# Optimization experiments

Hardware: AMD Instinct MI355X
Metric: run time of the kernel (lower is better)

Reference implementation:

```python
import jax, jax.numpy as jnp
import numpy as np

S, B, E, H = 2048, 4, 1024, 16
HD = E // H
EPS = 1e-8


def _bit_linear(x, W, b):
    """BitNetLinear (eval): ternary weight quant + abs-mean activation scaling."""
    w_scale = jnp.maximum(jnp.mean(jnp.abs(W)), EPS)
    wn = W / w_scale
    qw = jnp.sign(wn) * (jnp.abs(wn) > 0.5).astype(x.dtype)  # {-1,0,1}
    a_scale = jnp.maximum(jnp.mean(jnp.abs(x)), EPS)
    out = (x / a_scale) @ (qw * w_scale).T + b
    return out * a_scale


def setup_inputs() -> dict:
    key = jax.random.key(0)
    ks = jax.random.split(key, 9)
    # xavier-uniform-ish init for [E,E] weights
    lim = float(np.sqrt(6.0 / (E + E)))
    def w(k):
        return jax.random.uniform(k, (E, E), jnp.float32, -lim, lim)
    return {
        "query": jax.random.normal(ks[0], (S, B, E), jnp.float32),
        "Wq": w(ks[1]), "bq": jnp.zeros((E,), jnp.float32),
        "Wk": w(ks[2]), "bk": jnp.zeros((E,), jnp.float32),
        "Wv": w(ks[3]), "bv": jnp.zeros((E,), jnp.float32),
        "Wo": w(ks[4]), "bo": jnp.zeros((E,), jnp.float32),
    }


def reference(query, Wq, bq, Wk, bk, Wv, bv, Wo, bo):
    q = _bit_linear(query, Wq, bq)  # [S,B,E]
    k = _bit_linear(query, Wk, bk)
    v = _bit_linear(query, Wv, bv)
    # [S,B,E] -> [B*H, S, HD]
    def split_heads(t):
        return t.reshape(S, B * H, HD).transpose(1, 0, 2)
    q, k, v = split_heads(q), split_heads(k), split_heads(v)
    scaling = HD ** -0.5
    scores = jnp.einsum("nqd,nkd->nqk", q, k) * scaling  # [B*H,S,S]
    probs = jax.nn.softmax(scores, axis=-1)
    attn = jnp.einsum("nqk,nkd->nqd", probs, v)  # [B*H,S,HD]
    attn = attn.transpose(1, 0, 2).reshape(S, B, E)
    out = _bit_linear(attn, Wo, bo)  # [S,B,E]
    # need_weights=True, average_attn_weights=True -> mean over heads
    attn_weights = probs.reshape(B, H, S, S).mean(axis=1)  # [B,S,S]
    return out, attn_weights
```

## Files before the change

### kernel.cpp

```cpp
#include <hip/hip_runtime.h>


typedef __bf16 bf16_t;
typedef __bf16 bf16x8 __attribute__((ext_vector_type(8)));
typedef float  f32x4  __attribute__((ext_vector_type(4)));

#define MFMA16(Af, Bf, Cv) __builtin_amdgcn_mfma_f32_16x16x32_bf16((Af), (Bf), (Cv), 0, 0, 0)
#define EXP2(x) __builtin_amdgcn_exp2f(x)

constexpr float LOG2E   = 1.4426950408889634f;
constexpr float SHIFT2  = 14.426950408889634f;
constexpr float QSCALE  = 0.125f * LOG2E;

__device__ __forceinline__ void gload16(const void* g, void* l) {
  __builtin_amdgcn_global_load_lds(
      (const __attribute__((address_space(1))) void*)g,
      (__attribute__((address_space(3))) void*)l, 16, 0, 0);
}

__device__ __forceinline__ void stage8k(const bf16_t* __restrict__ g0, int gstride,
                                        char* ldsb, int tid, int w) {
  const int rr = tid >> 3;
  const int cs = ((tid & 7) * 8) ^ ((rr & 7) * 8);
  gload16(g0 + (size_t)rr * gstride + cs, ldsb + w * 1024);
  gload16(g0 + (size_t)(rr + 32) * gstride + cs, ldsb + 4096 + w * 1024);
}

__device__ __forceinline__ void stage8k512(const bf16_t* __restrict__ g0, int gstride,
                                           char* ldsb, int tid) {
  const int rr = tid >> 3;
  const int cs = ((tid & 7) * 8) ^ ((rr & 7) * 8);
  gload16(g0 + (size_t)rr * gstride + cs, ldsb + (tid >> 6) * 1024);
}

__device__ __forceinline__ bf16x8 lds_frag(const char* ldsb, int row, int bytecol) {
  return *(const bf16x8*)(ldsb + row * 128 + (bytecol ^ ((row & 7) << 4)));
}

constexpr int S_ = 2048, B_ = 4, E_ = 1024, H_ = 16, HD_ = 64;
constexpr int M_ = S_ * B_;
constexpr int NH_ = B_ * H_;

constexpr size_t OFF_SCALES = 0;
constexpr size_t OFF_PART   = 256;
constexpr size_t OFF_XB     = 8192;
constexpr size_t SZ_X       = (size_t)M_ * E_ * 2;
constexpr size_t OFF_TQKV   = OFF_XB + SZ_X;
constexpr size_t OFF_TO     = OFF_TQKV + (size_t)3072 * 1024 * 2;
constexpr size_t OFF_QH     = OFF_TO + (size_t)1024 * 1024 * 2;
constexpr size_t SZ_HD      = (size_t)NH_ * S_ * HD_ * 2;
constexpr size_t OFF_KH     = OFF_QH + SZ_HD;
constexpr size_t OFF_VT     = OFF_KH + SZ_HD;
constexpr size_t OFF_STL    = OFF_VT + SZ_HD;
constexpr size_t OFF_ATTN   = OFF_STL + (size_t)NH_ * S_ * 4;

__global__ void k_abs_sum_w4(const float4* __restrict__ W0, const float4* __restrict__ W1,
                             const float4* __restrict__ W2, const float4* __restrict__ W3,
                             float* __restrict__ part) {
  const int seg = blockIdx.x >> 8, blk = blockIdx.x & 255;
  const float4* src = (seg == 0) ? W0 : (seg == 1) ? W1 : (seg == 2) ? W2 : W3;
  float s = 0.f;
  for (int i = blk * 256 + threadIdx.x; i < 262144; i += 65536) {
    float4 x = src[i];
    s += fabsf(x.x) + fabsf(x.y) + fabsf(x.z) + fabsf(x.w);
  }
  __shared__ float red[256];
  red[threadIdx.x] = s; __syncthreads();
  for (int st = 128; st > 0; st >>= 1) {
    if (threadIdx.x < st) red[threadIdx.x] += red[threadIdx.x + st];
    __syncthreads();
  }
  if (threadIdx.x == 0) part[seg * 256 + blk] = red[0];
}

__global__ void k_prep_x(const float4* __restrict__ X, ushort4* __restrict__ Xb,
                         float* __restrict__ part) {
  float s = 0.f;
  for (int i = blockIdx.x * 256 + threadIdx.x; i < 2097152; i += 65536) {
    float4 v = X[i];
    s += fabsf(v.x) + fabsf(v.y) + fabsf(v.z) + fabsf(v.w);
    ushort4 h;
    h.x = __builtin_bit_cast(unsigned short, (__bf16)v.x);
    h.y = __builtin_bit_cast(unsigned short, (__bf16)v.y);
    h.z = __builtin_bit_cast(unsigned short, (__bf16)v.z);
    h.w = __builtin_bit_cast(unsigned short, (__bf16)v.w);
    Xb[i] = h;
  }
  __shared__ float red[256];
  red[threadIdx.x] = s; __syncthreads();
  for (int st = 128; st > 0; st >>= 1) {
    if (threadIdx.x < st) red[threadIdx.x] += red[threadIdx.x + st];
    __syncthreads();
  }
  if (threadIdx.x == 0) part[blockIdx.x] = red[0];
}

__global__ void k_abs_sum_bf16(const bf16x8* __restrict__ src, int n8, float* __restrict__ out) {
  float s = 0.f;
  for (int i = blockIdx.x * blockDim.x + threadIdx.x; i < n8; i += gridDim.x * blockDim.x) {
    bf16x8 x = src[i];
    #pragma unroll
    for (int e = 0; e < 8; ++e) s += fabsf((float)x[e]);
  }
  __shared__ float red[256];
  red[threadIdx.x] = s; __syncthreads();
  for (int st = 128; st > 0; st >>= 1) {
    if (threadIdx.x < st) red[threadIdx.x] += red[threadIdx.x + st];
    __syncthreads();
  }
  if (threadIdx.x == 0) out[blockIdx.x] = red[0];
}

__global__ void k_finalize(const float* __restrict__ part, float* __restrict__ scales,
                           int r0, int r1) {
  __shared__ float red[256];
  int t = threadIdx.x;
  for (int r = r0; r < r1; ++r) {
    red[t] = part[r * 256 + t];
    __syncthreads();
    for (int st = 128; st > 0; st >>= 1) {
      if (t < st) red[t] += red[t + st];
      __syncthreads();
    }
    if (t == 0) {
      float cnt = (r < 4) ? 1048576.0f : 8388608.0f;
      scales[r] = fmaxf(red[0] / cnt, 1e-8f);
    }
    __syncthreads();
  }
}

__device__ __forceinline__ unsigned short tern_u(float w, float wsc) {
  float wn = w / wsc;
  if (!(fabsf(wn) > 0.5f)) return 0;
  return (wn > 0.f) ? (unsigned short)0x3F80 : (unsigned short)0xBF80;
}

__global__ void k_quantize4(const float4* __restrict__ W0, const float4* __restrict__ W1,
                            const float4* __restrict__ W2, const float4* __restrict__ W3,
                            const float* __restrict__ scales,
                            ushort4* __restrict__ T0, ushort4* __restrict__ T1,
                            ushort4* __restrict__ T2, ushort4* __restrict__ T3) {
  const int seg = blockIdx.x >> 10;
  const int i = (blockIdx.x & 1023) * 256 + threadIdx.x;
  const float4* W = (seg == 0) ? W0 : (seg == 1) ? W1 : (seg == 2) ? W2 : W3;
  ushort4* T = (seg == 0) ? T0 : (seg == 1) ? T1 : (seg == 2) ? T2 : T3;
  float wsc = scales[seg];
  float4 w = W[i];
  ushort4 o;
  o.x = tern_u(w.x, wsc); o.y = tern_u(w.y, wsc);
  o.z = tern_u(w.z, wsc); o.w = tern_u(w.w, wsc);
  T[i] = o;
}

__global__ __launch_bounds__(256) void k_gemm_qkv(
    const bf16_t* __restrict__ Xb, const bf16_t* __restrict__ T,
    const float* __restrict__ scales,
    const float* __restrict__ bq, const float* __restrict__ bk, const float* __restrict__ bv,
    bf16_t* __restrict__ Qh, bf16_t* __restrict__ Kh, bf16_t* __restrict__ Vt) {
  __shared__ char lds[32768];
  const int tid = threadIdx.x, w = tid >> 6, lane = tid & 63;
  const int g = lane >> 4, cc = lane & 15;
  const int l = blockIdx.x;
  const int xcd = l & 7, r = l >> 3;
  const int nIdx = r % 24, mloc = r / 24;
  const int bm = (xcd * 8 + mloc) * 128, bn = nIdx * 128;
  const int wm = (w >> 1) * 64, wn = (w & 1) * 64;
  const int subA = wm >> 6, subB = wn >> 6;
  f32x4 acc[4][4] = {};
  for (int kt = 0; kt < 16; ++kt) {
    const int k0 = kt * 64;
    const bf16_t* xa = &Xb[(size_t)bm * 1024 + k0];
    const bf16_t* tb = &T[(size_t)bn * 1024 + k0];
    stage8k(xa, 1024, lds, tid, w);
    stage8k(xa + 64 * 1024, 1024, lds + 8192, tid, w);
    stage8k(tb, 1024, lds + 16384, tid, w);
    stage8k(tb + 64 * 1024, 1024, lds + 24576, tid, w);
    __syncthreads();
    const char* As = lds + subA * 8192;
    const char* Bs = lds + 16384 + subB * 8192;
    #pragma unroll
    for (int ks = 0; ks < 2; ++ks) {
      bf16x8 af[4], bfr[4];
      #pragma unroll
      for (int i = 0; i < 4; ++i)
        af[i] = lds_frag(As, (wm & 63) + i * 16 + cc, ks * 64 + g * 16);
      #pragma unroll
      for (int j = 0; j < 4; ++j)
        bfr[j] = lds_frag(Bs, (wn & 63) + j * 16 + cc, ks * 64 + g * 16);
      __builtin_amdgcn_s_setprio(1);
      #pragma unroll
      for (int i = 0; i < 4; ++i)
        #pragma unroll
        for (int j = 0; j < 4; ++j)
          acc[i][j] = MFMA16(af[i], bfr[j], acc[i][j]);
      __builtin_amdgcn_s_setprio(0);
    }
    __syncthreads();
  }
  const int seg = bn >> 10;
  const float wsc = scales[seg];
  const float asx = scales[4];
  const float* bias = (seg == 0) ? bq : (seg == 1) ? bk : bv;
  #pragma unroll
  for (int i = 0; i < 4; ++i)
    #pragma unroll
    for (int j = 0; j < 4; ++j)
      #pragma unroll
      for (int r2 = 0; r2 < 4; ++r2) {
        int m = bm + wm + i * 16 + g * 4 + r2;
        int n = bn + wn + j * 16 + cc;
        int e = n & 1023;
        float v = acc[i][j][r2] * wsc + bias[e] * asx;
        int s = m >> 2, b = m & 3, h = e >> 6, d = e & 63;
        if (seg == 0) {
          Qh[((b * 16 + h) * 2048 + s) * 64 + d] = (bf16_t)(v * QSCALE);
        } else if (seg == 1) {
          Kh[((b * 16 + h) * 2048 + s) * 64 + d] = (bf16_t)v;
        } else {
          Vt[((b * 16 + h) * 64 + d) * 2048 + s] = (bf16_t)v;
        }
      }
}

__global__ __launch_bounds__(512) void k_flash(
    const bf16_t* __restrict__ Qh, const bf16_t* __restrict__ Kh,
    const bf16_t* __restrict__ Vt,
    bf16_t* __restrict__ attnb, float* __restrict__ stl) {
  __shared__ char lds[81920];
  char* Ps = lds + 49152;
  const int tid = threadIdx.x, w = tid >> 6, lane = tid & 63;
  const int g = lane >> 4, cc = lane & 15;
  const int l = blockIdx.x;
  const int head = (l & 7) * 8 + ((l >> 3) & 7);
  const int q0 = (l >> 6) * 256;
  const int qbaseA = (head * 2048 + q0 + w * 32 + cc) * 64 + g * 8;
  const int qbaseB = qbaseA + 16 * 64;
  const bf16x8 qa0 = *(const bf16x8*)&Qh[qbaseA];
  const bf16x8 qa1 = *(const bf16x8*)&Qh[qbaseA + 32];
  const bf16x8 qb0 = *(const bf16x8*)&Qh[qbaseB];
  const bf16x8 qb1 = *(const bf16x8*)&Qh[qbaseB + 32];
  const bf16_t* Kb = Kh + (size_t)head * 2048 * 64;
  const bf16_t* Vb = Vt + (size_t)head * 64 * 2048;
  const bf16_t one_b = (bf16_t)1.0f;
  const bf16x8 ones = {one_b, one_b, one_b, one_b, one_b, one_b, one_b, one_b};
  const f32x4 minit = {-SHIFT2, -SHIFT2, -SHIFT2, -SHIFT2};
  f32x4 accOA[4] = {}, accOB[4] = {};
  f32x4 accLA = {}, accLB = {};
  stage8k512(Kb, 64, lds, tid);
  stage8k512(Vb, 2048, lds + 24576, tid);
  stage8k512(Kb + 64 * 64, 64, lds + 8192, tid);
  stage8k512(Vb + 64, 2048, lds + 24576 + 8192, tid);
  int cur = 0;
  for (int t = 0; t < 32; ++t) {
    if (t < 31) asm volatile("s_waitcnt vmcnt(2)" ::: "memory");
    else        asm volatile("s_waitcnt vmcnt(0)" ::: "memory");
    __builtin_amdgcn_s_barrier();
    if (t + 2 < 32) {
      int nb = cur + 2; if (nb >= 3) nb -= 3;
      stage8k512(Kb + (t + 2) * 64 * 64, 64, lds + nb * 8192, tid);
      stage8k512(Vb + (t + 2) * 64, 2048, lds + 24576 + nb * 8192, tid);
    }
    const char* KhL = lds + cur * 8192;
    const char* VtL = lds + 24576 + cur * 8192;
    f32x4 sA[4], sB[4];
    #pragma unroll
    for (int nf = 0; nf < 4; ++nf) { sA[nf] = minit; sB[nf] = minit; }
    __builtin_amdgcn_s_setprio(1);
    #pragma unroll
    for (int nf = 0; nf < 4; ++nf) {
      const int row = nf * 16 + cc;
      bf16x8 kh0 = lds_frag(KhL, row, g * 16);
      bf16x8 kh1 = lds_frag(KhL, row, 64 + g * 16);
      sA[nf] = MFMA16(qa0, kh0, sA[nf]);
      sA[nf] = MFMA16(qa1, kh1, sA[nf]);
      sB[nf] = MFMA16(qb0, kh0, sB[nf]);
      sB[nf] = MFMA16(qb1, kh1, sB[nf]);
    }
    __builtin_amdgcn_s_setprio(0);
    #pragma unroll
    for (int nf = 0; nf < 4; ++nf)
      #pragma unroll
      for (int r = 0; r < 4; ++r) {
        float pA = EXP2(sA[nf][r]);
        float pB = EXP2(sB[nf][r]);
        int rowA = w * 32 + g * 4 + r;
        int rowB = rowA + 16;
        int colb = (nf * 16 + cc) * 2;
        *(bf16_t*)(Ps + ((rowA * 128 + colb) ^ ((rowA & 7) << 4))) = (bf16_t)pA;
        *(bf16_t*)(Ps + ((rowB * 128 + colb) ^ ((rowB & 7) << 4))) = (bf16_t)pB;
      }
    const int prA = w * 32 + cc, prB = prA + 16;
    const int pbA = (prA * 128 + g * 16) ^ ((prA & 7) << 4);
    const int pbB = (prB * 128 + g * 16) ^ ((prB & 7) << 4);
    const bf16x8 paA0 = *(const bf16x8*)(Ps + pbA);
    const bf16x8 paA1 = *(const bf16x8*)(Ps + (pbA ^ 64));
    const bf16x8 paB0 = *(const bf16x8*)(Ps + pbB);
    const bf16x8 paB1 = *(const bf16x8*)(Ps + (pbB ^ 64));
    __builtin_amdgcn_s_setprio(1);
    accLA = MFMA16(paA0, ones, accLA);
    accLA = MFMA16(paA1, ones, accLA);
    accLB = MFMA16(paB0, ones, accLB);
    accLB = MFMA16(paB1, ones, accLB);
    #pragma unroll
    for (int df = 0; df < 4; ++df) {
      const int row = df * 16 + cc;
      bf16x8 v0 = lds_frag(VtL, row, g * 16);
      bf16x8 v1 = lds_frag(VtL, row, 64 + g * 16);
      accOA[df] = MFMA16(paA0, v0, accOA[df]);
      accOA[df] = MFMA16(paA1, v1, accOA[df]);
      accOB[df] = MFMA16(paB0, v0, accOB[df]);
      accOB[df] = MFMA16(paB1, v1, accOB[df]);
    }
    __builtin_amdgcn_s_setprio(0);
    cur = cur + 1; if (cur >= 3) cur = 0;
  }
  const int b = head >> 4, h = head & 15;
  #pragma unroll
  for (int df = 0; df < 4; ++df)
    #pragma unroll
    for (int r = 0; r < 4; ++r) {
      int qA = q0 + w * 32 + g * 4 + r;
      int e = h * 64 + df * 16 + cc;
      attnb[(qA * 4 + b) * 1024 + e] = (bf16_t)(accOA[df][r] / accLA[r]);
      attnb[((qA + 16) * 4 + b) * 1024 + e] = (bf16_t)(accOB[df][r] / accLB[r]);
    }
  if (cc == 0) {
    #pragma unroll
    for (int r = 0; r < 4; ++r) {
      int qA = q0 + w * 32 + g * 4 + r;
      stl[head * 2048 + qA] = accLA[r];
      stl[head * 2048 + qA + 16] = accLB[r];
    }
  }
}

__global__ __launch_bounds__(256) void k_pm(
    const bf16_t* __restrict__ Qh, const bf16_t* __restrict__ Kh,
    const float* __restrict__ stl, float* __restrict__ aw) {
  __shared__ char kbuf[2 * 16384];
  __shared__ float sc_[2048];
  const int tid = threadIdx.x, w = tid >> 6, lane = tid & 63;
  const int g = lane >> 4, cc = lane & 15;
  const int l = blockIdx.x;
  const int q0 = (l & 15) * 128, b = (l >> 4) & 3, z = l >> 6;
  const int kbeg = z * 128;
  for (int i = tid; i < 2048; i += 256) {
    int h = i >> 7, q = i & 127;
    sc_[i] = -log2f(stl[(b * 16 + h) * 2048 + q0 + q]) - SHIFT2;
  }
  __syncthreads();
  stage8k(Kh + ((size_t)(b * 16 + 0) * 2048 + kbeg) * 64, 64, kbuf, tid, w);
  stage8k(Kh + ((size_t)(b * 16 + 1) * 2048 + kbeg) * 64, 64, kbuf + 8192, tid, w);
  int cur = 0;
  float pmA[4][4], pmB[4][4];
  for (int it = 0; it < 16; ++it) {
    const int kt = it >> 3, hp = it & 7;
    const int ktl = kbeg + kt * 64;
    asm volatile("s_waitcnt vmcnt(0)" ::: "memory");
    __builtin_amdgcn_s_barrier();
    if (it + 1 < 16) {
      const int nx = it + 1;
      const int ktn = kbeg + (nx >> 3) * 64, hpn = nx & 7;
      char* nb = kbuf + (cur ^ 1) * 16384;
      stage8k(Kh + ((size_t)(b * 16 + 2 * hpn) * 2048 + ktn) * 64, 64, nb, tid, w);
      stage8k(Kh + ((size_t)(b * 16 + 2 * hpn + 1) * 2048 + ktn) * 64, 64, nb + 8192, tid, w);
    }
    if (hp == 0) {
      #pragma unroll
      for (int nf = 0; nf < 4; ++nf)
        #pragma unroll
        for (int r = 0; r < 4; ++r) { pmA[nf][r] = 0.f; pmB[nf][r] = 0.f; }
    }
    #pragma unroll
    for (int hi = 0; hi < 2; ++hi) {
      const int h = 2 * hp + hi;
      const int head = b * 16 + h;
      const int qbaseA = (head * 2048 + q0 + w * 32 + cc) * 64 + g * 8;
      const int qbaseB = qbaseA + 16 * 64;
      bf16x8 qa0 = *(const bf16x8*)&Qh[qbaseA];
      bf16x8 qa1 = *(const bf16x8*)&Qh[qbaseA + 32];
      bf16x8 qb0 = *(const bf16x8*)&Qh[qbaseB];
      bf16x8 qb1 = *(const bf16x8*)&Qh[qbaseB + 32];
      f32x4 ciA, ciB;
      #pragma unroll
      for (int r = 0; r < 4; ++r) {
        int qloc = w * 32 + g * 4 + r;
        ciA[r] = sc_[h * 128 + qloc];
        ciB[r] = sc_[h * 128 + qloc + 16];
      }
      const char* KhL = kbuf + cur * 16384 + hi * 8192;
      f32x4 sA[4], sB[4];
      #pragma unroll
      for (int nf = 0; nf < 4; ++nf) { sA[nf] = ciA; sB[nf] = ciB; }
      __builtin_amdgcn_s_setprio(1);
      #pragma unroll
      for (int nf = 0; nf < 4; ++nf) {
        const int row = nf * 16 + cc;
        bf16x8 kh0 = lds_frag(KhL, row, g * 16);
        bf16x8 kh1 = lds_frag(KhL, row, 64 + g * 16);
        sA[nf] = MFMA16(qa0, kh0, sA[nf]);
        sA[nf] = MFMA16(qa1, kh1, sA[nf]);
        sB[nf] = MFMA16(qb0, kh0, sB[nf]);
        sB[nf] = MFMA16(qb1, kh1, sB[nf]);
      }
      __builtin_amdgcn_s_setprio(0);
      #pragma unroll
      for (int nf = 0; nf < 4; ++nf)
        #pragma unroll
        for (int r = 0; r < 4; ++r) {
          pmA[nf][r] += EXP2(sA[nf][r]);
          pmB[nf][r] += EXP2(sB[nf][r]);
        }
    }
    if (hp == 7) {
      #pragma unroll
      for (int nf = 0; nf < 4; ++nf)
        #pragma unroll
        for (int r = 0; r < 4; ++r) {
          int qA = q0 + w * 32 + g * 4 + r;
          int k = ktl + nf * 16 + cc;
          aw[((long)(b * 2048 + qA)) * 2048 + k] = pmA[nf][r] * 0.0625f;
          aw[((long)(b * 2048 + qA + 16)) * 2048 + k] = pmB[nf][r] * 0.0625f;
        }
    }
    cur ^= 1;
  }
}

__global__ __launch_bounds__(256) void k_gemm_out(
    const bf16_t* __restrict__ A, const bf16_t* __restrict__ T,
    const float* __restrict__ scales, const float* __restrict__ bo,
    float* __restrict__ out) {
  __shared__ char lds[32768];
  const int tid = threadIdx.x, w = tid >> 6, lane = tid & 63;
  const int g = lane >> 4, cc = lane & 15;
  const int l = blockIdx.x;
  const int xcd = l & 7, r = l >> 3;
  const int nIdx = r & 7, mloc = r >> 3;
  const int bm = (xcd * 8 + mloc) * 128, bn = nIdx * 128;
  const int wm = (w >> 1) * 64, wn = (w & 1) * 64;
  const int subA = wm >> 6, subB = wn >> 6;
  f32x4 acc[4][4] = {};
  for (int kt = 0; kt < 16; ++kt) {
    const int k0 = kt * 64;
    const bf16_t* aa = &A[(size_t)bm * 1024 + k0];
    const bf16_t* tb = &T[(size_t)bn * 1024 + k0];
    stage8k(aa, 1024, lds, tid, w);
    stage8k(aa + 64 * 1024, 1024, lds + 8192, tid, w);
    stage8k(tb, 1024, lds + 16384, tid, w);
    stage8k(tb + 64 * 1024, 1024, lds + 24576, tid, w);
    __syncthreads();
    const char* As = lds + subA * 8192;
    const char* Bs = lds + 16384 + subB * 8192;
    #pragma unroll
    for (int ks = 0; ks < 2; ++ks) {
      bf16x8 af[4], bfr[4];
      #pragma unroll
      for (int i = 0; i < 4; ++i)
        af[i] = lds_frag(As, (wm & 63) + i * 16 + cc, ks * 64 + g * 16);
      #pragma unroll
      for (int j = 0; j < 4; ++j)
        bfr[j] = lds_frag(Bs, (wn & 63) + j * 16 + cc, ks * 64 + g * 16);
      __builtin_amdgcn_s_setprio(1);
      #pragma unroll
      for (int i = 0; i < 4; ++i)
        #pragma unroll
        for (int j = 0; j < 4; ++j)
          acc[i][j] = MFMA16(af[i], bfr[j], acc[i][j]);
      __builtin_amdgcn_s_setprio(0);
    }
    __syncthreads();
  }
  const float wsc = scales[3], asa = scales[5];
  #pragma unroll
  for (int i = 0; i < 4; ++i)
    #pragma unroll
    for (int j = 0; j < 4; ++j)
      #pragma unroll
      for (int r2 = 0; r2 < 4; ++r2) {
        int m = bm + wm + i * 16 + g * 4 + r2;
        int n = bn + wn + j * 16 + cc;
        out[m * 1024 + n] = acc[i][j][r2] * wsc + bo[n] * asa;
      }
}

extern "C" void kernel_launch(void* const* d_in, const int* in_sizes, int n_in,
                              void* d_out, int out_size, void* d_ws, size_t ws_size,
                              hipStream_t stream) {
  (void)in_sizes; (void)n_in; (void)out_size; (void)ws_size;
  const float* query = (const float*)d_in[0];
  const float* Wq = (const float*)d_in[1];
  const float* bq = (const float*)d_in[2];
  const float* Wk = (const float*)d_in[3];
  const float* bk = (const float*)d_in[4];
  const float* Wv = (const float*)d_in[5];
  const float* bv = (const float*)d_in[6];
  const float* Wo = (const float*)d_in[7];
  const float* bo = (const float*)d_in[8];

  char* ws = (char*)d_ws;
  float*  scales = (float*)(ws + OFF_SCALES);
  float*  part   = (float*)(ws + OFF_PART);
  bf16_t* Xb     = (bf16_t*)(ws + OFF_XB);
  bf16_t* Tqkv   = (bf16_t*)(ws + OFF_TQKV);
  bf16_t* To     = (bf16_t*)(ws + OFF_TO);
  bf16_t* Qh     = (bf16_t*)(ws + OFF_QH);
  bf16_t* Kh     = (bf16_t*)(ws + OFF_KH);
  bf16_t* Vt     = (bf16_t*)(ws + OFF_VT);
  float*  Stl    = (float*)(ws + OFF_STL);
  bf16_t* Attn   = (bf16_t*)(ws + OFF_ATTN);

  float* out0 = (float*)d_out;
  float* aw   = out0 + (size_t)M_ * E_;

  k_abs_sum_w4<<<1024, 256, 0, stream>>>((const float4*)Wq, (const float4*)Wk,
                                         (const float4*)Wv, (const float4*)Wo, part);
  k_prep_x<<<256, 256, 0, stream>>>((const float4*)query, (ushort4*)Xb, part + 1024);
  k_finalize<<<1, 256, 0, stream>>>(part, scales, 0, 5);
  k_quantize4<<<4096, 256, 0, stream>>>((const float4*)Wq, (const float4*)Wk,
                                        (const float4*)Wv, (const float4*)Wo, scales,
                                        (ushort4*)Tqkv, (ushort4*)(Tqkv + 1048576),
                                        (ushort4*)(Tqkv + 2097152), (ushort4*)To);

  k_gemm_qkv<<<1536, 256, 0, stream>>>(Xb, Tqkv, scales, bq, bk, bv, Qh, Kh, Vt);
  k_flash<<<512, 512, 0, stream>>>(Qh, Kh, Vt, Attn, Stl);
  k_pm<<<1024, 256, 0, stream>>>(Qh, Kh, Stl, aw);
  k_abs_sum_bf16<<<256, 256, 0, stream>>>((const bf16x8*)Attn, 1048576, part + 1280);
  k_finalize<<<1, 256, 0, stream>>>(part, scales, 5, 6);
  k_gemm_out<<<512, 256, 0, stream>>>(Attn, To, scales, bo, out0);
}
```

Before: 309.6 us.

## Rewrite flash attention with 32x32 MFMA and register-resident P via permlane swap

The flash kernel moves from 16x16x32 to 32x32x16 bf16 MFMA and computes the transposed score tile (K as A operand, Q as B), so the probabilities already sit in registers in a layout usable as the A operand of the PV product after packed bf16 conversion and permlane32 swaps. This removes the LDS round trip for P: the 32KB P buffer, its scattered stores and reloads and the extra LDS footprint are gone, and a launch-bounds occupancy hint is added. It adds cross-lane permutes and new packing and index logic that must match the MFMA layouts, and the 16-float accumulators may raise register pressure.

```diff
diff --git a/kernel.cpp b/kernel.cpp
--- a/kernel.cpp
+++ b/kernel.cpp
@@ -4,13 +4,23 @@
 typedef __bf16 bf16_t;
 typedef __bf16 bf16x8 __attribute__((ext_vector_type(8)));
 typedef float  f32x4  __attribute__((ext_vector_type(4)));
+typedef float  f32x16 __attribute__((ext_vector_type(16)));
+typedef unsigned u32x2 __attribute__((ext_vector_type(2)));
+typedef unsigned u32x4 __attribute__((ext_vector_type(4)));
 
 #define MFMA16(Af, Bf, Cv) __builtin_amdgcn_mfma_f32_16x16x32_bf16((Af), (Bf), (Cv), 0, 0, 0)
+#define MFMA32(Af, Bf, Cv) __builtin_amdgcn_mfma_f32_32x32x16_bf16((Af), (Bf), (Cv), 0, 0, 0)
 #define EXP2(x) __builtin_amdgcn_exp2f(x)
 
 constexpr float LOG2E   = 1.4426950408889634f;
 constexpr float SHIFT2  = 14.426950408889634f;
 constexpr float QSCALE  = 0.125f * LOG2E;
+
+__device__ __forceinline__ unsigned cvt_pk_bf16(float lo, float hi) {
+  unsigned r;
+  asm("v_cvt_pk_bf16_f32 %0, %1, %2" : "=v"(r) : "v"(lo), "v"(hi));
+  return r;
+}
 
 __device__ __forceinline__ void gload16(const void* g, void* l) {
   __builtin_amdgcn_global_load_lds(
@@ -223,30 +233,25 @@
       }
 }
 
-__global__ __launch_bounds__(512) void k_flash(
+__global__ __launch_bounds__(512, 4) void k_flash(
     const bf16_t* __restrict__ Qh, const bf16_t* __restrict__ Kh,
     const bf16_t* __restrict__ Vt,
     bf16_t* __restrict__ attnb, float* __restrict__ stl) {
-  __shared__ char lds[81920];
-  char* Ps = lds + 49152;
+  __shared__ char lds[49152];
   const int tid = threadIdx.x, w = tid >> 6, lane = tid & 63;
-  const int g = lane >> 4, cc = lane & 15;
+  const int h5 = lane >> 5, c31 = lane & 31;
   const int l = blockIdx.x;
   const int head = (l & 7) * 8 + ((l >> 3) & 7);
   const int q0 = (l >> 6) * 256;
-  const int qbaseA = (head * 2048 + q0 + w * 32 + cc) * 64 + g * 8;
-  const int qbaseB = qbaseA + 16 * 64;
-  const bf16x8 qa0 = *(const bf16x8*)&Qh[qbaseA];
-  const bf16x8 qa1 = *(const bf16x8*)&Qh[qbaseA + 32];
-  const bf16x8 qb0 = *(const bf16x8*)&Qh[qbaseB];
-  const bf16x8 qb1 = *(const bf16x8*)&Qh[qbaseB + 32];
+  const bf16_t* Qp = &Qh[((size_t)head * 2048 + q0 + w * 32 + c31) * 64];
+  bf16x8 qr[8];
+  #pragma unroll
+  for (int j = 0; j < 8; ++j) qr[j] = *(const bf16x8*)&Qp[j * 8];
   const bf16_t* Kb = Kh + (size_t)head * 2048 * 64;
   const bf16_t* Vb = Vt + (size_t)head * 64 * 2048;
   const bf16_t one_b = (bf16_t)1.0f;
   const bf16x8 ones = {one_b, one_b, one_b, one_b, one_b, one_b, one_b, one_b};
-  const f32x4 minit = {-SHIFT2, -SHIFT2, -SHIFT2, -SHIFT2};
-  f32x4 accOA[4] = {}, accOB[4] = {};
-  f32x4 accLA = {}, accLB = {};
+  f32x16 accO0 = {}, accO1 = {}, accL = {};
   stage8k512(Kb, 64, lds, tid);
   stage8k512(Vb, 2048, lds + 24576, tid);
   stage8k512(Kb + 64 * 64, 64, lds + 8192, tid);
@@ -263,74 +268,59 @@
     }
     const char* KhL = lds + cur * 8192;
     const char* VtL = lds + 24576 + cur * 8192;
-    f32x4 sA[4], sB[4];
-    #pragma unroll
-    for (int nf = 0; nf < 4; ++nf) { sA[nf] = minit; sB[nf] = minit; }
-    __builtin_amdgcn_s_setprio(1);
-    #pragma unroll
-    for (int nf = 0; nf < 4; ++nf) {
-      const int row = nf * 16 + cc;
-      bf16x8 kh0 = lds_frag(KhL, row, g * 16);
-      bf16x8 kh1 = lds_frag(KhL, row, 64 + g * 16);
-      sA[nf] = MFMA16(qa0, kh0, sA[nf]);
-      sA[nf] = MFMA16(qa1, kh1, sA[nf]);
-      sB[nf] = MFMA16(qb0, kh0, sB[nf]);
-      sB[nf] = MFMA16(qb1, kh1, sB[nf]);
-    }
-    __builtin_amdgcn_s_setprio(0);
-    #pragma unroll
-    for (int nf = 0; nf < 4; ++nf)
-      #pragma unroll
-      for (int r = 0; r < 4; ++r) {
-        float pA = EXP2(sA[nf][r]);
-        float pB = EXP2(sB[nf][r]);
-        int rowA = w * 32 + g * 4 + r;
-        int rowB = rowA + 16;
-        int colb = (nf * 16 + cc) * 2;
-        *(bf16_t*)(Ps + ((rowA * 128 + colb) ^ ((rowA & 7) << 4))) = (bf16_t)pA;
-        *(bf16_t*)(Ps + ((rowB * 128 + colb) ^ ((rowB & 7) << 4))) = (bf16_t)pB;
-      }
-    const int prA = w * 32 + cc, prB = prA + 16;
-    const int pbA = (prA * 128 + g * 16) ^ ((prA & 7) << 4);
-    const int pbB = (prB * 128 + g * 16) ^ ((prB & 7) << 4);
-    const bf16x8 paA0 = *(const bf16x8*)(Ps + pbA);
-    const bf16x8 paA1 = *(const bf16x8*)(Ps + (pbA ^ 64));
-    const bf16x8 paB0 = *(const bf16x8*)(Ps + pbB);
-    const bf16x8 paB1 = *(const bf16x8*)(Ps + (pbB ^ 64));
-    __builtin_amdgcn_s_setprio(1);
-    accLA = MFMA16(paA0, ones, accLA);
-    accLA = MFMA16(paA1, ones, accLA);
-    accLB = MFMA16(paB0, ones, accLB);
-    accLB = MFMA16(paB1, ones, accLB);
-    #pragma unroll
-    for (int df = 0; df < 4; ++df) {
-      const int row = df * 16 + cc;
-      bf16x8 v0 = lds_frag(VtL, row, g * 16);
-      bf16x8 v1 = lds_frag(VtL, row, 64 + g * 16);
-      accOA[df] = MFMA16(paA0, v0, accOA[df]);
-      accOA[df] = MFMA16(paA1, v1, accOA[df]);
-      accOB[df] = MFMA16(paB0, v0, accOB[df]);
-      accOB[df] = MFMA16(paB1, v1, accOB[df]);
-    }
-    __builtin_amdgcn_s_setprio(0);
+    #pragma unroll
+    for (int kb = 0; kb < 2; ++kb) {
+      f32x16 s;
+      #pragma unroll
+      for (int i = 0; i < 16; ++i) s[i] = -SHIFT2;
+      __builtin_amdgcn_s_setprio(1);
+      #pragma unroll
+      for (int m = 0; m < 4; ++m) {
+        bf16x8 kf = lds_frag(KhL, kb * 32 + c31, m * 32 + h5 * 16);
+        s = MFMA32(kf, qr[m * 2 + h5], s);
+      }
+      __builtin_amdgcn_s_setprio(0);
+      float p[16];
+      #pragma unroll
+      for (int i = 0; i < 16; ++i) p[i] = EXP2(s[i]);
+      unsigned pk[4][2];
+      #pragma unroll
+      for (int m = 0; m < 4; ++m) {
+        pk[m][0] = cvt_pk_bf16(p[4 * m], p[4 * m + 1]);
+        pk[m][1] = cvt_pk_bf16(p[4 * m + 2], p[4 * m + 3]);
+      }
+      #pragma unroll
+      for (int n = 0; n < 2; ++n) {
+        u32x2 s0 = __builtin_amdgcn_permlane32_swap(pk[2 * n][0], pk[2 * n + 1][0], false, false);
+        u32x2 s1 = __builtin_amdgcn_permlane32_swap(pk[2 * n][1], pk[2 * n + 1][1], false, false);
+        u32x4 fw = {s0[0], s1[0], s0[1], s1[1]};
+        bf16x8 pf = __builtin_bit_cast(bf16x8, fw);
+        bf16x8 v0 = lds_frag(VtL, c31, kb * 64 + n * 32 + h5 * 16);
+        bf16x8 v1 = lds_frag(VtL, 32 + c31, kb * 64 + n * 32 + h5 * 16);
+        __builtin_amdgcn_s_setprio(1);
+        accL = MFMA32(pf, ones, accL);
+        accO0 = MFMA32(pf, v0, accO0);
+        accO1 = MFMA32(pf, v1, accO1);
+        __builtin_amdgcn_s_setprio(0);
+      }
+    }
     cur = cur + 1; if (cur >= 3) cur = 0;
   }
-  const int b = head >> 4, h = head & 15;
+  const int b = head >> 4, hh = head & 15;
   #pragma unroll
-  for (int df = 0; df < 4; ++df)
-    #pragma unroll
-    for (int r = 0; r < 4; ++r) {
-      int qA = q0 + w * 32 + g * 4 + r;
-      int e = h * 64 + df * 16 + cc;
-      attnb[(qA * 4 + b) * 1024 + e] = (bf16_t)(accOA[df][r] / accLA[r]);
-      attnb[((qA + 16) * 4 + b) * 1024 + e] = (bf16_t)(accOB[df][r] / accLB[r]);
-    }
-  if (cc == 0) {
-    #pragma unroll
-    for (int r = 0; r < 4; ++r) {
-      int qA = q0 + w * 32 + g * 4 + r;
-      stl[head * 2048 + qA] = accLA[r];
-      stl[head * 2048 + qA + 16] = accLB[r];
+  for (int r = 0; r < 16; ++r) {
+    int qrw = (r & 3) + 8 * (r >> 2) + 4 * h5;
+    int q = q0 + w * 32 + qrw;
+    int m = q * 4 + b;
+    float il = 1.0f / accL[r];
+    attnb[(size_t)m * 1024 + hh * 64 + c31] = (bf16_t)(accO0[r] * il);
+    attnb[(size_t)m * 1024 + hh * 64 + 32 + c31] = (bf16_t)(accO1[r] * il);
+  }
+  if (c31 == 0) {
+    #pragma unroll
+    for (int r = 0; r < 16; ++r) {
+      int qrw = (r & 3) + 8 * (r >> 2) + 4 * h5;
+      stl[head * 2048 + q0 + w * 32 + qrw] = accL[r];
     }
   }
 }
```

Result: slower. 319.9 us (+3.3%).
